# Optimization experiments

Hardware: AMD Instinct MI355X
Metric: run time of the kernel (lower is better)

The kernel has to match this reference:

```python
import jax, jax.numpy as jnp
import numpy as np

N = 50000      # nodes
E = 1600000    # edges (avg degree 32)
G = 128        # graphs in batch
NE = 5         # spectral supports (edge_attr channels)
NIN = 16       # input node features
H = 64         # nout1 hidden width
NCLS = 6
BN_EPS = 1e-5


def setup_inputs() -> dict:
    key = jax.random.key(0)
    ks = jax.random.split(key, 12)
    s = 0.1  # weight init scale
    x = jax.random.normal(ks[0], (N, NIN), dtype=jnp.float32)
    edge_index = jax.random.randint(ks[1], (2, E), 0, N, dtype=jnp.int32)
    edge_attr = jax.random.normal(ks[2], (E, NE), dtype=jnp.float32)
    # sorted segment ids covering all G graphs (non-empty segments)
    batch = ((jnp.arange(N, dtype=jnp.int32) * G) // N).astype(jnp.int32)
    W1 = jax.random.normal(ks[3], (NE, NIN, H), dtype=jnp.float32) * s
    W2 = jax.random.normal(ks[4], (NE, H, H), dtype=jnp.float32) * s
    W3 = jax.random.normal(ks[5], (NE, H, H), dtype=jnp.float32) * s
    W4 = jax.random.normal(ks[6], (NE, H, H), dtype=jnp.float32) * s
    b1 = jnp.zeros((H,), jnp.float32)
    b2 = jnp.zeros((H,), jnp.float32)
    b3 = jnp.zeros((H,), jnp.float32)
    b4 = jnp.zeros((H,), jnp.float32)
    bn_gamma = jnp.ones((2 * H,), jnp.float32)
    bn_beta = jnp.zeros((2 * H,), jnp.float32)
    bn_mean = jax.random.normal(ks[7], (2 * H,), dtype=jnp.float32)
    bn_var = jax.random.uniform(ks[8], (2 * H,), dtype=jnp.float32) + 0.5
    fc_w = jax.random.normal(ks[9], (2 * H, NCLS), dtype=jnp.float32) * s
    fc_b = jnp.zeros((NCLS,), jnp.float32)
    return {"x": x, "edge_index": edge_index, "edge_attr": edge_attr,
            "batch": batch, "W1": W1, "b1": b1, "W2": W2, "b2": b2,
            "W3": W3, "b3": b3, "W4": W4, "b4": b4,
            "bn_gamma": bn_gamma, "bn_beta": bn_beta,
            "bn_mean": bn_mean, "bn_var": bn_var,
            "fc_w": fc_w, "fc_b": fc_b}


def spect_conv(x, src, dst, edge_attr, W, b):
    # SpectConv(selfconn=False): out = sum_k scatter_add(edge_attr[:,k]*x[src] -> dst) @ W[k] + b
    xs = x[src]  # [E, F] gather
    n = x.shape[0]
    out = jnp.zeros((n, W.shape[2]), x.dtype)
    for k in range(W.shape[0]):  # K=5 spectral supports
        h = jax.ops.segment_sum(edge_attr[:, k:k + 1] * xs, dst, num_segments=n)
        out = out + h @ W[k]
    return out + b


def reference(x, edge_index, edge_attr, batch, W1, b1, W2, b2, W3, b3, W4, b4,
              bn_gamma, bn_beta, bn_mean, bn_var, fc_w, fc_b):
    src, dst = edge_index[0], edge_index[1]
    h = jax.nn.relu(spect_conv(x, src, dst, edge_attr, W1, b1))
    h = jax.nn.relu(spect_conv(h, src, dst, edge_attr, W2, b2))
    h = jax.nn.relu(spect_conv(h, src, dst, edge_attr, W3, b3))
    h = jax.nn.relu(spect_conv(h, src, dst, edge_attr, W4, b4))
    pooled = jnp.concatenate([
        jax.ops.segment_sum(h, batch, num_segments=G),
        jax.ops.segment_max(h, batch, num_segments=G)], axis=1)  # [G, 2H]
    bn = (pooled - bn_mean) * jax.lax.rsqrt(bn_var + BN_EPS) * bn_gamma + bn_beta
    return jax.nn.log_softmax(bn @ fc_w + fc_b, axis=1)
```

## Files before the change

### kernel.cpp

```cpp
#include <hip/hip_runtime.h>


#define Nn   50000
#define Ne   1600000
#define Gg   128
#define NEk  5
#define NINf 16
#define NCLSo 6
#define NB   196

using short8 = __attribute__((ext_vector_type(8))) short;
using f32x4  = __attribute__((ext_vector_type(4))) float;

__device__ __forceinline__ float2 bf2u(unsigned u) {
    return make_float2(__uint_as_float(u << 16), __uint_as_float(u & 0xffff0000u));
}
__device__ __forceinline__ unsigned f2bf(float a, float b) {
    unsigned ua = __float_as_uint(a), ub = __float_as_uint(b);
    ua += 0x7fffu + ((ua >> 16) & 1u);
    ub += 0x7fffu + ((ub >> 16) & 1u);
    return (ua >> 16) | (ub & 0xffff0000u);
}
__device__ __forceinline__ unsigned short f2bf1(float a) {
    unsigned ua = __float_as_uint(a);
    ua += 0x7fffu + ((ua >> 16) & 1u);
    return (unsigned short)(ua >> 16);
}


__global__ void k_pad_x(const float* __restrict__ x, unsigned* __restrict__ h0) {
    int i = blockIdx.x * 256 + threadIdx.x;
    if (i >= Nn * 32) return;
    int n = i >> 5, p = i & 31;
    int f0 = 2 * p;
    float v0 = (f0 < NINf) ? x[n * NINf + f0] : 0.f;
    float v1 = (f0 + 1 < NINf) ? x[n * NINf + f0 + 1] : 0.f;
    h0[i] = f2bf(v0, v1);
}

__global__ void k_pad_w1(const float* __restrict__ W1, float* __restrict__ W1p) {
    int i = blockIdx.x * 256 + threadIdx.x;
    if (i >= NEk * 64 * 64) return;
    int h = i & 63, f = (i >> 6) & 63, k = i >> 12;
    W1p[i] = (f < NINf) ? W1[(k * NINf + f) * 64 + h] : 0.f;
}

__global__ void k_pack_b(const float* __restrict__ W, unsigned short* __restrict__ bhi,
                         unsigned short* __restrict__ blo) {
    int i = blockIdx.x * 256 + threadIdx.x;
    if (i >= 20480) return;
    int j = i & 7, lane = (i >> 3) & 63, t2 = i >> 9;
    int nt = t2 / 10, kstep = t2 - nt * 10;
    int k = kstep * 32 + (lane >> 4) * 8 + j;
    int col = nt * 16 + (lane & 15);
    float v = W[k * 64 + col];
    unsigned short hi = f2bf1(v);
    float fhi = __uint_as_float(((unsigned)hi) << 16);
    bhi[i] = hi;
    blo[i] = f2bf1(v - fhi);
}

__global__ void k_rank(const int* __restrict__ ei, int* __restrict__ deg,
                       int* __restrict__ rank) {
    int e = blockIdx.x * 256 + threadIdx.x;
    if (e >= Ne) return;
    rank[e] = atomicAdd(&deg[ei[Ne + e]], 1);
}


__global__ void k_blocksum(const int* __restrict__ deg, int* __restrict__ bsum) {
    __shared__ int l[256];
    int t = threadIdx.x;
    int i = blockIdx.x * 256 + t;
    l[t] = (i < Nn) ? deg[i] : 0;
    __syncthreads();
    for (int off = 128; off > 0; off >>= 1) {
        if (t < off) l[t] += l[t + off];
        __syncthreads();
    }
    if (t == 0) bsum[blockIdx.x] = l[0];
}

__global__ void k_scanpart(const int* __restrict__ bsum, int* __restrict__ boff) {
    __shared__ int l[256];
    int t = threadIdx.x;
    int v = (t < NB) ? bsum[t] : 0;
    l[t] = v;
    __syncthreads();
    for (int off = 1; off < 256; off <<= 1) {
        int u = (t >= off) ? l[t - off] : 0;
        __syncthreads();
        l[t] += u;
        __syncthreads();
    }
    if (t < NB) boff[t] = l[t] - v;
}

__global__ void k_scanfinal(const int* __restrict__ deg, const int* __restrict__ boff,
                            int* __restrict__ rowstart) {
    __shared__ int l[256];
    int t = threadIdx.x;
    int i = blockIdx.x * 256 + t;
    int v = (i < Nn) ? deg[i] : 0;
    l[t] = v;
    __syncthreads();
    for (int off = 1; off < 256; off <<= 1) {
        int u = (t >= off) ? l[t - off] : 0;
        __syncthreads();
        l[t] += u;
        __syncthreads();
    }
    if (i <= Nn) rowstart[i] = boff[blockIdx.x] + l[t] - v;
}

__global__ void k_place(const int* __restrict__ ei, const float* __restrict__ eattr,
                        const int* __restrict__ rowstart, const int* __restrict__ rank,
                        uint4* __restrict__ recs) {
    int e = blockIdx.x * 256 + threadIdx.x;
    if (e >= Ne) return;
    int d = ei[Ne + e];
    int pos = rowstart[d] + rank[e];
    const float* a = eattr + (size_t)e * 5;
    uint4 r;
    r.x = (unsigned)ei[e];
    r.y = f2bf(a[0], a[1]);
    r.z = f2bf(a[2], a[3]);
    r.w = f2bf(a[4], 0.f);
    recs[pos] = r;
}

__global__ void k_bounds(const int* __restrict__ batch, int* __restrict__ sg,
                         int* __restrict__ eg) {
    int n = blockIdx.x * 256 + threadIdx.x;
    if (n >= Nn) return;
    int g = batch[n];
    if (n == 0) sg[g] = 0;
    else {
        int gp = batch[n - 1];
        if (gp != g) { sg[g] = n; eg[gp] = n; }
    }
    if (n == Nn - 1) eg[g] = Nn;
}


__global__ __launch_bounds__(256) void k_aggregate(
    const unsigned* __restrict__ hin, const int* __restrict__ rowstart,
    const uint4* __restrict__ recs, unsigned* __restrict__ agg) {
    int lane = threadIdx.x & 63;
    int l = lane & 31, half = lane >> 5;
    int node = __builtin_amdgcn_readfirstlane((int)(blockIdx.x * 4 + (threadIdx.x >> 6)));
    int beg = rowstart[node], end = rowstart[node + 1];
    float2 c0 = {0.f, 0.f}, c1 = c0, c2 = c0, c3 = c0, c4 = c0;
    int ee = beg;
#define EDGE(E) { \
    uint4 r = recs[(E)]; \
    unsigned hx = hin[(size_t)(int)r.x * 32 + l]; \
    float2 xv = bf2u(hx); \
    float2 A01 = bf2u(r.y), A23 = bf2u(r.z); \
    float a4v = __uint_as_float(r.w << 16); \
    c0.x = fmaf(A01.x, xv.x, c0.x); c0.y = fmaf(A01.x, xv.y, c0.y); \
    c1.x = fmaf(A01.y, xv.x, c1.x); c1.y = fmaf(A01.y, xv.y, c1.y); \
    c2.x = fmaf(A23.x, xv.x, c2.x); c2.y = fmaf(A23.x, xv.y, c2.y); \
    c3.x = fmaf(A23.y, xv.x, c3.x); c3.y = fmaf(A23.y, xv.y, c3.y); \
    c4.x = fmaf(a4v,  xv.x, c4.x); c4.y = fmaf(a4v,  xv.y, c4.y); }
    for (; ee + 8 <= end; ee += 8) {
        EDGE(ee + half) EDGE(ee + 2 + half) EDGE(ee + 4 + half) EDGE(ee + 6 + half)
    }
    for (; ee + 2 <= end; ee += 2) { EDGE(ee + half) }
    if (ee < end) { if (half == 0) { EDGE(ee) } }
#undef EDGE
    c0.x += __shfl(c0.x, lane ^ 32); c0.y += __shfl(c0.y, lane ^ 32);
    c1.x += __shfl(c1.x, lane ^ 32); c1.y += __shfl(c1.y, lane ^ 32);
    c2.x += __shfl(c2.x, lane ^ 32); c2.y += __shfl(c2.y, lane ^ 32);
    c3.x += __shfl(c3.x, lane ^ 32); c3.y += __shfl(c3.y, lane ^ 32);
    c4.x += __shfl(c4.x, lane ^ 32); c4.y += __shfl(c4.y, lane ^ 32);
    if (half == 0) {
        unsigned* o = agg + (size_t)node * 160 + l;
        o[0]   = f2bf(c0.x, c0.y);
        o[32]  = f2bf(c1.x, c1.y);
        o[64]  = f2bf(c2.x, c2.y);
        o[96]  = f2bf(c3.x, c3.y);
        o[128] = f2bf(c4.x, c4.y);
    }
}

#define SPAD 41
__global__ __launch_bounds__(256) void k_transform(
    const uint4* __restrict__ A, const unsigned short* __restrict__ bhi,
    const unsigned short* __restrict__ blo, const float* __restrict__ bias,
    unsigned* __restrict__ outh) {
    __shared__ uint4 smem[64 * SPAD];
    int t = threadIdx.x;
    int lane = t & 63, wave = t >> 6;
    int m = lane & 15, quad = lane >> 4;
    int blk = blockIdx.x;

#pragma unroll
    for (int it = 0; it < 10; ++it) {
        int v = t + it * 256;
        int row = v / 40, off = v - row * 40;
        int node = blk * 64 + row;
        if (node >= Nn) node = Nn - 1;
        smem[row * SPAD + off] = A[(size_t)node * 40 + off];
    }
    __syncthreads();

    f32x4 acc0 = {0.f, 0.f, 0.f, 0.f}, acc1 = acc0, acc2 = acc0, acc3 = acc0;
    const uint4* arow = smem + (wave * 16 + m) * SPAD + quad;
#pragma unroll 2
    for (int ks = 0; ks < 10; ++ks) {
        short8 a = *(const short8*)(arow + ks * 4);
        size_t bb = ((size_t)ks * 64 + lane) * 8;
        short8 h0 = *(const short8*)(bhi + bb);
        short8 l0 = *(const short8*)(blo + bb);
        acc0 = __builtin_amdgcn_mfma_f32_16x16x32_bf16(a, h0, acc0, 0, 0, 0);
        acc0 = __builtin_amdgcn_mfma_f32_16x16x32_bf16(a, l0, acc0, 0, 0, 0);
        short8 h1 = *(const short8*)(bhi + bb + 5120);
        short8 l1 = *(const short8*)(blo + bb + 5120);
        acc1 = __builtin_amdgcn_mfma_f32_16x16x32_bf16(a, h1, acc1, 0, 0, 0);
        acc1 = __builtin_amdgcn_mfma_f32_16x16x32_bf16(a, l1, acc1, 0, 0, 0);
        short8 h2 = *(const short8*)(bhi + bb + 10240);
        short8 l2 = *(const short8*)(blo + bb + 10240);
        acc2 = __builtin_amdgcn_mfma_f32_16x16x32_bf16(a, h2, acc2, 0, 0, 0);
        acc2 = __builtin_amdgcn_mfma_f32_16x16x32_bf16(a, l2, acc2, 0, 0, 0);
        short8 h3 = *(const short8*)(bhi + bb + 15360);
        short8 l3 = *(const short8*)(blo + bb + 15360);
        acc3 = __builtin_amdgcn_mfma_f32_16x16x32_bf16(a, h3, acc3, 0, 0, 0);
        acc3 = __builtin_amdgcn_mfma_f32_16x16x32_bf16(a, l3, acc3, 0, 0, 0);
    }
    __syncthreads();

    float* Cs = (float*)smem;
#pragma unroll
    for (int r = 0; r < 4; ++r) {
        int base = wave * 1152 + (quad * 4 + r) * 72 + m;
        Cs[base]      = acc0[r];
        Cs[base + 16] = acc1[r];
        Cs[base + 32] = acc2[r];
        Cs[base + 48] = acc3[r];
    }
    __syncthreads();

    int row = t >> 2, grp = t & 3;
    int node = blk * 64 + row;
    if (node < Nn) {
        const float* cr = Cs + (row >> 4) * 1152 + (row & 15) * 72;
        unsigned o[8];
#pragma unroll
        for (int j = 0; j < 8; ++j) {
            int pp = grp * 8 + j;
            float v0 = fmaxf(cr[2 * pp]     + bias[2 * pp],     0.f);
            float v1 = fmaxf(cr[2 * pp + 1] + bias[2 * pp + 1], 0.f);
            o[j] = f2bf(v0, v1);
        }
        uint4* dst = (uint4*)(outh + (size_t)node * 32 + grp * 8);
        dst[0] = make_uint4(o[0], o[1], o[2], o[3]);
        dst[1] = make_uint4(o[4], o[5], o[6], o[7]);
    }
}


__global__ __launch_bounds__(256) void k_pool(const unsigned* __restrict__ h,
                                              const int* __restrict__ sg,
                                              const int* __restrict__ eg,
                                              float* __restrict__ pooled) {
    __shared__ float2 ls[256], lm[256];
    int g = blockIdx.x, t = threadIdx.x;
    int p = t & 31, q = t >> 5;
    int s = sg[g], e = eg[g];
    float2 sum = {0.f, 0.f}, mx = {0.f, 0.f};
    for (int n = s + q; n < e; n += 8) {
        float2 v = bf2u(h[(size_t)n * 32 + p]);
        sum.x += v.x; sum.y += v.y;
        mx.x = fmaxf(mx.x, v.x); mx.y = fmaxf(mx.y, v.y);
    }
    ls[t] = sum; lm[t] = mx;
    __syncthreads();
    if (t < 32) {
        float2 ss = ls[t], mm = lm[t];
        for (int i = 1; i < 8; ++i) {
            float2 a = ls[t + i * 32], b = lm[t + i * 32];
            ss.x += a.x; ss.y += a.y;
            mm.x = fmaxf(mm.x, b.x); mm.y = fmaxf(mm.y, b.y);
        }
        pooled[g * 128 + 2 * t]          = ss.x;
        pooled[g * 128 + 2 * t + 1]      = ss.y;
        pooled[g * 128 + 64 + 2 * t]     = mm.x;
        pooled[g * 128 + 64 + 2 * t + 1] = mm.y;
    }
}

__global__ void k_head(const float* __restrict__ pooled, const float* __restrict__ gamma,
                       const float* __restrict__ beta, const float* __restrict__ mean,
                       const float* __restrict__ var, const float* __restrict__ fcw,
                       const float* __restrict__ fcb, float* __restrict__ out) {
    __shared__ float y[128];
    __shared__ float lg[8];
    int g = blockIdx.x, c = threadIdx.x;
    float p = pooled[g * 128 + c];
    y[c] = (p - mean[c]) * rsqrtf(var[c] + 1e-5f) * gamma[c] + beta[c];
    __syncthreads();
    if (c < NCLSo) {
        float l = fcb[c];
        for (int i = 0; i < 128; ++i) l += y[i] * fcw[i * NCLSo + c];
        lg[c] = l;
    }
    __syncthreads();
    if (c == 0) {
        float m = lg[0];
        for (int j = 1; j < NCLSo; ++j) m = fmaxf(m, lg[j]);
        float se = 0.f;
        for (int j = 0; j < NCLSo; ++j) se += expf(lg[j] - m);
        float lse = m + logf(se);
        for (int j = 0; j < NCLSo; ++j) out[g * NCLSo + j] = lg[j] - lse;
    }
}


static inline size_t rup(size_t x) { return (x + 255) & ~(size_t)255; }

extern "C" void kernel_launch(void* const* d_in, const int* in_sizes, int n_in,
                              void* d_out, int out_size, void* d_ws, size_t ws_size,
                              hipStream_t stream) {
    const float* x     = (const float*)d_in[0];
    const int*   ei    = (const int*)d_in[1];
    const float* eattr = (const float*)d_in[2];
    const int*   batch = (const int*)d_in[3];
    const float* W1    = (const float*)d_in[4];
    const float* b1    = (const float*)d_in[5];
    const float* W2    = (const float*)d_in[6];
    const float* b2    = (const float*)d_in[7];
    const float* W3    = (const float*)d_in[8];
    const float* b3    = (const float*)d_in[9];
    const float* W4    = (const float*)d_in[10];
    const float* b4    = (const float*)d_in[11];
    const float* gamma = (const float*)d_in[12];
    const float* beta  = (const float*)d_in[13];
    const float* mean  = (const float*)d_in[14];
    const float* var   = (const float*)d_in[15];
    const float* fcw   = (const float*)d_in[16];
    const float* fcb   = (const float*)d_in[17];
    float* out = (float*)d_out;

    char* p = (char*)d_ws;
    auto take = [&](size_t bytes) { char* r = p; p += rup(bytes); return r; };
    int*            deg      = (int*)take((size_t)(Nn + 1) * 4);
    int*            rowstart = (int*)take((size_t)(Nn + 1) * 4);
    int*            bsum     = (int*)take((size_t)NB * 4);
    int*            boff     = (int*)take((size_t)NB * 4);
    int*            rank     = (int*)take((size_t)Ne * 4);
    uint4*          recs     = (uint4*)take((size_t)Ne * 16);
    unsigned*       hA       = (unsigned*)take((size_t)Nn * 32 * 4);
    unsigned*       hB       = (unsigned*)take((size_t)Nn * 32 * 4);
    unsigned*       agg      = (unsigned*)take((size_t)Nn * 160 * 4);
    float*          W1p      = (float*)take((size_t)NEk * 64 * 64 * 4);
    unsigned short* bhiA     = (unsigned short*)take((size_t)4 * 20480 * 2);
    unsigned short* bloA     = (unsigned short*)take((size_t)4 * 20480 * 2);
    float*          pooled   = (float*)take((size_t)Gg * 128 * 4);
    int*            sg       = (int*)take((size_t)Gg * 4);
    int*            eg       = (int*)take((size_t)Gg * 4);

    hipMemsetAsync(deg, 0, (size_t)(Nn + 1) * 4, stream);

    k_pad_x<<<(Nn * 32 + 255) / 256, 256, 0, stream>>>(x, hA);
    k_pad_w1<<<(NEk * 64 * 64 + 255) / 256, 256, 0, stream>>>(W1, W1p);
    k_pack_b<<<80, 256, 0, stream>>>(W1p, bhiA,             bloA);
    k_pack_b<<<80, 256, 0, stream>>>(W2,  bhiA + 20480,     bloA + 20480);
    k_pack_b<<<80, 256, 0, stream>>>(W3,  bhiA + 2 * 20480, bloA + 2 * 20480);
    k_pack_b<<<80, 256, 0, stream>>>(W4,  bhiA + 3 * 20480, bloA + 3 * 20480);
    k_rank<<<(Ne + 255) / 256, 256, 0, stream>>>(ei, deg, rank);
    k_blocksum<<<NB, 256, 0, stream>>>(deg, bsum);
    k_scanpart<<<1, 256, 0, stream>>>(bsum, boff);
    k_scanfinal<<<NB, 256, 0, stream>>>(deg, boff, rowstart);
    k_place<<<(Ne + 255) / 256, 256, 0, stream>>>(ei, eattr, rowstart, rank, recs);
    k_bounds<<<(Nn + 255) / 256, 256, 0, stream>>>(batch, sg, eg);

    const float* bs[4] = { b1, b2, b3, b4 };
    unsigned* cur = hA;
    unsigned* nxt = hB;
    for (int L = 0; L < 4; ++L) {
        k_aggregate<<<Nn / 4, 256, 0, stream>>>(cur, rowstart, recs, agg);
        k_transform<<<(Nn + 63) / 64, 256, 0, stream>>>(
            (const uint4*)agg, bhiA + (size_t)L * 20480, bloA + (size_t)L * 20480,
            bs[L], nxt);
        unsigned* tmp = cur; cur = nxt; nxt = tmp;
    }

    k_pool<<<Gg, 256, 0, stream>>>(cur, sg, eg, pooled);
    k_head<<<Gg, 128, 0, stream>>>(pooled, gamma, beta, mean, var, fcw, fcb, out);
}
```

Before: 525.6 us.

## Fuse aggregation and MFMA transform into one per-layer kernel; pad degree counters

Merges the edge aggregation kernel and the bf16 MFMA transform into a single 512-thread kernel per layer. Each block aggregates 64 nodes straight into LDS, then multiplies them by the packed weights, so the 160-wide aggregate buffer no longer makes a round trip through global memory. Separately, the degree counters are spaced 64 bytes apart to cut atomic contention and false sharing in the rank pass. The trade-offs are less aggregation parallelism per block (each wave handles 8 nodes serially), a barrier that makes the MFMA stage wait for the slowest node's gather, and a 16x larger degree array to memset.

```diff
diff --git a/kernel.cpp b/kernel.cpp
--- a/kernel.cpp
+++ b/kernel.cpp
@@ -8,6 +8,7 @@
 #define NINf 16
 #define NCLSo 6
 #define NB   196
+#define SPAD 41
 
 using short8 = __attribute__((ext_vector_type(8))) short;
 using f32x4  = __attribute__((ext_vector_type(4))) float;
@@ -64,7 +65,7 @@
                        int* __restrict__ rank) {
     int e = blockIdx.x * 256 + threadIdx.x;
     if (e >= Ne) return;
-    rank[e] = atomicAdd(&deg[ei[Ne + e]], 1);
+    rank[e] = atomicAdd(&deg[ei[Ne + e] * 16], 1);
 }
 
 
@@ -72,7 +73,7 @@
     __shared__ int l[256];
     int t = threadIdx.x;
     int i = blockIdx.x * 256 + t;
-    l[t] = (i < Nn) ? deg[i] : 0;
+    l[t] = (i < Nn) ? deg[i * 16] : 0;
     __syncthreads();
     for (int off = 128; off > 0; off >>= 1) {
         if (t < off) l[t] += l[t + off];
@@ -101,7 +102,7 @@
     __shared__ int l[256];
     int t = threadIdx.x;
     int i = blockIdx.x * 256 + t;
-    int v = (i < Nn) ? deg[i] : 0;
+    int v = (i < Nn) ? deg[i * 16] : 0;
     l[t] = v;
     __syncthreads();
     for (int off = 1; off < 256; off <<= 1) {
@@ -142,16 +143,24 @@
     if (n == Nn - 1) eg[g] = Nn;
 }
 
-
-__global__ __launch_bounds__(256) void k_aggregate(
+__global__ __launch_bounds__(512) void k_layer(
     const unsigned* __restrict__ hin, const int* __restrict__ rowstart,
-    const uint4* __restrict__ recs, unsigned* __restrict__ agg) {
-    int lane = threadIdx.x & 63;
+    const uint4* __restrict__ recs, const unsigned short* __restrict__ bhi,
+    const unsigned short* __restrict__ blo, const float* __restrict__ bias,
+    unsigned* __restrict__ outh) {
+    __shared__ uint4 smem[64 * SPAD];
+    int t = threadIdx.x;
+    int lane = t & 63, wave = t >> 6;
     int l = lane & 31, half = lane >> 5;
-    int node = __builtin_amdgcn_readfirstlane((int)(blockIdx.x * 4 + (threadIdx.x >> 6)));
-    int beg = rowstart[node], end = rowstart[node + 1];
-    float2 c0 = {0.f, 0.f}, c1 = c0, c2 = c0, c3 = c0, c4 = c0;
-    int ee = beg;
+    unsigned* As = (unsigned*)smem;
+
+    for (int i = 0; i < 8; ++i) {
+        int row = wave * 8 + i;
+        int node = __builtin_amdgcn_readfirstlane(blockIdx.x * 64 + row);
+        float2 c0 = {0.f, 0.f}, c1 = c0, c2 = c0, c3 = c0, c4 = c0;
+        if (node < Nn) {
+            int beg = rowstart[node], end = rowstart[node + 1];
+            int ee = beg;
 #define EDGE(E) { \
     uint4 r = recs[(E)]; \
     unsigned hx = hin[(size_t)(int)r.x * 32 + l]; \
@@ -163,99 +172,71 @@
     c2.x = fmaf(A23.x, xv.x, c2.x); c2.y = fmaf(A23.x, xv.y, c2.y); \
     c3.x = fmaf(A23.y, xv.x, c3.x); c3.y = fmaf(A23.y, xv.y, c3.y); \
     c4.x = fmaf(a4v,  xv.x, c4.x); c4.y = fmaf(a4v,  xv.y, c4.y); }
-    for (; ee + 8 <= end; ee += 8) {
-        EDGE(ee + half) EDGE(ee + 2 + half) EDGE(ee + 4 + half) EDGE(ee + 6 + half)
-    }
-    for (; ee + 2 <= end; ee += 2) { EDGE(ee + half) }
-    if (ee < end) { if (half == 0) { EDGE(ee) } }
+            for (; ee + 8 <= end; ee += 8) {
+                EDGE(ee + half) EDGE(ee + 2 + half) EDGE(ee + 4 + half) EDGE(ee + 6 + half)
+            }
+            for (; ee + 2 <= end; ee += 2) { EDGE(ee + half) }
+            if (ee < end) { if (half == 0) { EDGE(ee) } }
 #undef EDGE
-    c0.x += __shfl(c0.x, lane ^ 32); c0.y += __shfl(c0.y, lane ^ 32);
-    c1.x += __shfl(c1.x, lane ^ 32); c1.y += __shfl(c1.y, lane ^ 32);
-    c2.x += __shfl(c2.x, lane ^ 32); c2.y += __shfl(c2.y, lane ^ 32);
-    c3.x += __shfl(c3.x, lane ^ 32); c3.y += __shfl(c3.y, lane ^ 32);
-    c4.x += __shfl(c4.x, lane ^ 32); c4.y += __shfl(c4.y, lane ^ 32);
-    if (half == 0) {
-        unsigned* o = agg + (size_t)node * 160 + l;
-        o[0]   = f2bf(c0.x, c0.y);
-        o[32]  = f2bf(c1.x, c1.y);
-        o[64]  = f2bf(c2.x, c2.y);
-        o[96]  = f2bf(c3.x, c3.y);
-        o[128] = f2bf(c4.x, c4.y);
-    }
-}
-
-#define SPAD 41
-__global__ __launch_bounds__(256) void k_transform(
-    const uint4* __restrict__ A, const unsigned short* __restrict__ bhi,
-    const unsigned short* __restrict__ blo, const float* __restrict__ bias,
-    unsigned* __restrict__ outh) {
-    __shared__ uint4 smem[64 * SPAD];
-    int t = threadIdx.x;
-    int lane = t & 63, wave = t >> 6;
+            c0.x += __shfl(c0.x, lane ^ 32); c0.y += __shfl(c0.y, lane ^ 32);
+            c1.x += __shfl(c1.x, lane ^ 32); c1.y += __shfl(c1.y, lane ^ 32);
+            c2.x += __shfl(c2.x, lane ^ 32); c2.y += __shfl(c2.y, lane ^ 32);
+            c3.x += __shfl(c3.x, lane ^ 32); c3.y += __shfl(c3.y, lane ^ 32);
+            c4.x += __shfl(c4.x, lane ^ 32); c4.y += __shfl(c4.y, lane ^ 32);
+        }
+        if (half == 0) {
+            unsigned* o = As + row * (SPAD * 4) + l;
+            o[0]   = f2bf(c0.x, c0.y);
+            o[32]  = f2bf(c1.x, c1.y);
+            o[64]  = f2bf(c2.x, c2.y);
+            o[96]  = f2bf(c3.x, c3.y);
+            o[128] = f2bf(c4.x, c4.y);
+        }
+    }
+    __syncthreads();
+
     int m = lane & 15, quad = lane >> 4;
-    int blk = blockIdx.x;
-
-#pragma unroll
-    for (int it = 0; it < 10; ++it) {
-        int v = t + it * 256;
-        int row = v / 40, off = v - row * 40;
-        int node = blk * 64 + row;
-        if (node >= Nn) node = Nn - 1;
-        smem[row * SPAD + off] = A[(size_t)node * 40 + off];
-    }
-    __syncthreads();
-
-    f32x4 acc0 = {0.f, 0.f, 0.f, 0.f}, acc1 = acc0, acc2 = acc0, acc3 = acc0;
-    const uint4* arow = smem + (wave * 16 + m) * SPAD + quad;
+    int mtile = wave & 3, np = wave >> 2;
+    f32x4 acc0 = {0.f, 0.f, 0.f, 0.f}, acc1 = acc0;
+    const uint4* arow = smem + (mtile * 16 + m) * SPAD + quad;
 #pragma unroll 2
     for (int ks = 0; ks < 10; ++ks) {
         short8 a = *(const short8*)(arow + ks * 4);
-        size_t bb = ((size_t)ks * 64 + lane) * 8;
-        short8 h0 = *(const short8*)(bhi + bb);
-        short8 l0 = *(const short8*)(blo + bb);
+        size_t b0 = ((size_t)((2 * np) * 10 + ks) * 64 + lane) * 8;
+        size_t b1 = ((size_t)((2 * np + 1) * 10 + ks) * 64 + lane) * 8;
+        short8 h0 = *(const short8*)(bhi + b0);
+        short8 l0 = *(const short8*)(blo + b0);
         acc0 = __builtin_amdgcn_mfma_f32_16x16x32_bf16(a, h0, acc0, 0, 0, 0);
         acc0 = __builtin_amdgcn_mfma_f32_16x16x32_bf16(a, l0, acc0, 0, 0, 0);
-        short8 h1 = *(const short8*)(bhi + bb + 5120);
-        short8 l1 = *(const short8*)(blo + bb + 5120);
+        short8 h1 = *(const short8*)(bhi + b1);
+        short8 l1 = *(const short8*)(blo + b1);
         acc1 = __builtin_amdgcn_mfma_f32_16x16x32_bf16(a, h1, acc1, 0, 0, 0);
         acc1 = __builtin_amdgcn_mfma_f32_16x16x32_bf16(a, l1, acc1, 0, 0, 0);
-        short8 h2 = *(const short8*)(bhi + bb + 10240);
-        short8 l2 = *(const short8*)(blo + bb + 10240);
-        acc2 = __builtin_amdgcn_mfma_f32_16x16x32_bf16(a, h2, acc2, 0, 0, 0);
-        acc2 = __builtin_amdgcn_mfma_f32_16x16x32_bf16(a, l2, acc2, 0, 0, 0);
-        short8 h3 = *(const short8*)(bhi + bb + 15360);
-        short8 l3 = *(const short8*)(blo + bb + 15360);
-        acc3 = __builtin_amdgcn_mfma_f32_16x16x32_bf16(a, h3, acc3, 0, 0, 0);
-        acc3 = __builtin_amdgcn_mfma_f32_16x16x32_bf16(a, l3, acc3, 0, 0, 0);
     }
     __syncthreads();
 
     float* Cs = (float*)smem;
 #pragma unroll
     for (int r = 0; r < 4; ++r) {
-        int base = wave * 1152 + (quad * 4 + r) * 72 + m;
-        Cs[base]      = acc0[r];
-        Cs[base + 16] = acc1[r];
-        Cs[base + 32] = acc2[r];
-        Cs[base + 48] = acc3[r];
-    }
-    __syncthreads();
-
-    int row = t >> 2, grp = t & 3;
-    int node = blk * 64 + row;
+        int row = mtile * 16 + quad * 4 + r;
+        Cs[row * 66 + (2 * np) * 16 + m]     = acc0[r];
+        Cs[row * 66 + (2 * np + 1) * 16 + m] = acc1[r];
+    }
+    __syncthreads();
+
+    int row = t >> 3, cg = t & 7;
+    int node = blockIdx.x * 64 + row;
     if (node < Nn) {
-        const float* cr = Cs + (row >> 4) * 1152 + (row & 15) * 72;
-        unsigned o[8];
+        const float* cr = Cs + row * 66 + cg * 8;
+        const float* bb = bias + cg * 8;
+        unsigned o[4];
 #pragma unroll
-        for (int j = 0; j < 8; ++j) {
-            int pp = grp * 8 + j;
-            float v0 = fmaxf(cr[2 * pp]     + bias[2 * pp],     0.f);
-            float v1 = fmaxf(cr[2 * pp + 1] + bias[2 * pp + 1], 0.f);
+        for (int j = 0; j < 4; ++j) {
+            float v0 = fmaxf(cr[2 * j]     + bb[2 * j],     0.f);
+            float v1 = fmaxf(cr[2 * j + 1] + bb[2 * j + 1], 0.f);
             o[j] = f2bf(v0, v1);
         }
-        uint4* dst = (uint4*)(outh + (size_t)node * 32 + grp * 8);
-        dst[0] = make_uint4(o[0], o[1], o[2], o[3]);
-        dst[1] = make_uint4(o[4], o[5], o[6], o[7]);
+        *(uint4*)(outh + (size_t)node * 32 + cg * 4) = make_uint4(o[0], o[1], o[2], o[3]);
     }
 }
 
@@ -344,7 +325,7 @@
 
     char* p = (char*)d_ws;
     auto take = [&](size_t bytes) { char* r = p; p += rup(bytes); return r; };
-    int*            deg      = (int*)take((size_t)(Nn + 1) * 4);
+    int*            deg      = (int*)take((size_t)(Nn + 1) * 64);
     int*            rowstart = (int*)take((size_t)(Nn + 1) * 4);
     int*            bsum     = (int*)take((size_t)NB * 4);
     int*            boff     = (int*)take((size_t)NB * 4);
@@ -352,7 +333,6 @@
     uint4*          recs     = (uint4*)take((size_t)Ne * 16);
     unsigned*       hA       = (unsigned*)take((size_t)Nn * 32 * 4);
     unsigned*       hB       = (unsigned*)take((size_t)Nn * 32 * 4);
-    unsigned*       agg      = (unsigned*)take((size_t)Nn * 160 * 4);
     float*          W1p      = (float*)take((size_t)NEk * 64 * 64 * 4);
     unsigned short* bhiA     = (unsigned short*)take((size_t)4 * 20480 * 2);
     unsigned short* bloA     = (unsigned short*)take((size_t)4 * 20480 * 2);
@@ -360,7 +340,7 @@
     int*            sg       = (int*)take((size_t)Gg * 4);
     int*            eg       = (int*)take((size_t)Gg * 4);
 
-    hipMemsetAsync(deg, 0, (size_t)(Nn + 1) * 4, stream);
+    hipMemsetAsync(deg, 0, (size_t)(Nn + 1) * 64, stream);
 
     k_pad_x<<<(Nn * 32 + 255) / 256, 256, 0, stream>>>(x, hA);
     k_pad_w1<<<(NEk * 64 * 64 + 255) / 256, 256, 0, stream>>>(W1, W1p);
@@ -379,9 +359,8 @@
     unsigned* cur = hA;
     unsigned* nxt = hB;
     for (int L = 0; L < 4; ++L) {
-        k_aggregate<<<Nn / 4, 256, 0, stream>>>(cur, rowstart, recs, agg);
-        k_transform<<<(Nn + 63) / 64, 256, 0, stream>>>(
-            (const uint4*)agg, bhiA + (size_t)L * 20480, bloA + (size_t)L * 20480,
+        k_layer<<<(Nn + 63) / 64, 512, 0, stream>>>(
+            cur, rowstart, recs, bhiA + (size_t)L * 20480, bloA + (size_t)L * 20480,
             bs[L], nxt);
         unsigned* tmp = cur; cur = nxt; nxt = tmp;
     }
```

Result: slower. 603.7 us (+14.8%).

## Split node features into two halves and aggregate each in a separate pass

Applied to the files above, without the earlier changes.

Node features are stored as two 32-feature bf16 arrays (lo/hi), and aggregation runs twice per layer, once per half. Each pass uses a 16-lane feature slice with four edges in flight per wave, so each gathered feature table is half the size and more likely to stay in cache. The edge records are read twice per layer, now with nontemporal loads. The degree counters are also spaced 64 bytes apart to reduce atomic contention on shared cache lines.

```diff
diff --git a/kernel.cpp b/kernel.cpp
--- a/kernel.cpp
+++ b/kernel.cpp
@@ -8,9 +8,11 @@
 #define NINf 16
 #define NCLSo 6
 #define NB   196
+#define SPAD 41
 
 using short8 = __attribute__((ext_vector_type(8))) short;
 using f32x4  = __attribute__((ext_vector_type(4))) float;
+using uint4v = __attribute__((ext_vector_type(4))) unsigned;
 
 __device__ __forceinline__ float2 bf2u(unsigned u) {
     return make_float2(__uint_as_float(u << 16), __uint_as_float(u & 0xffff0000u));
@@ -28,14 +30,17 @@
 }
 
 
-__global__ void k_pad_x(const float* __restrict__ x, unsigned* __restrict__ h0) {
+__global__ void k_pad_x(const float* __restrict__ x, unsigned* __restrict__ hLo,
+                        unsigned* __restrict__ hHi) {
     int i = blockIdx.x * 256 + threadIdx.x;
     if (i >= Nn * 32) return;
     int n = i >> 5, p = i & 31;
     int f0 = 2 * p;
     float v0 = (f0 < NINf) ? x[n * NINf + f0] : 0.f;
     float v1 = (f0 + 1 < NINf) ? x[n * NINf + f0 + 1] : 0.f;
-    h0[i] = f2bf(v0, v1);
+    unsigned v = f2bf(v0, v1);
+    if (p < 16) hLo[n * 16 + p] = v;
+    else        hHi[n * 16 + (p - 16)] = v;
 }
 
 __global__ void k_pad_w1(const float* __restrict__ W1, float* __restrict__ W1p) {
@@ -64,7 +69,7 @@
                        int* __restrict__ rank) {
     int e = blockIdx.x * 256 + threadIdx.x;
     if (e >= Ne) return;
-    rank[e] = atomicAdd(&deg[ei[Ne + e]], 1);
+    rank[e] = atomicAdd(&deg[ei[Ne + e] * 16], 1);
 }
 
 
@@ -72,7 +77,7 @@
     __shared__ int l[256];
     int t = threadIdx.x;
     int i = blockIdx.x * 256 + t;
-    l[t] = (i < Nn) ? deg[i] : 0;
+    l[t] = (i < Nn) ? deg[i * 16] : 0;
     __syncthreads();
     for (int off = 128; off > 0; off >>= 1) {
         if (t < off) l[t] += l[t + off];
@@ -101,7 +106,7 @@
     __shared__ int l[256];
     int t = threadIdx.x;
     int i = blockIdx.x * 256 + t;
-    int v = (i < Nn) ? deg[i] : 0;
+    int v = (i < Nn) ? deg[i * 16] : 0;
     l[t] = v;
     __syncthreads();
     for (int off = 1; off < 256; off <<= 1) {
@@ -143,18 +148,18 @@
 }
 
 
-__global__ __launch_bounds__(256) void k_aggregate(
+__global__ __launch_bounds__(256) void k_aggregate_half(
     const unsigned* __restrict__ hin, const int* __restrict__ rowstart,
-    const uint4* __restrict__ recs, unsigned* __restrict__ agg) {
+    const uint4v* __restrict__ recs, unsigned* __restrict__ agg, int halfSel) {
     int lane = threadIdx.x & 63;
-    int l = lane & 31, half = lane >> 5;
+    int l = lane & 15, q = lane >> 4;
     int node = __builtin_amdgcn_readfirstlane((int)(blockIdx.x * 4 + (threadIdx.x >> 6)));
     int beg = rowstart[node], end = rowstart[node + 1];
     float2 c0 = {0.f, 0.f}, c1 = c0, c2 = c0, c3 = c0, c4 = c0;
     int ee = beg;
 #define EDGE(E) { \
-    uint4 r = recs[(E)]; \
-    unsigned hx = hin[(size_t)(int)r.x * 32 + l]; \
+    uint4v r = __builtin_nontemporal_load(&recs[(E)]); \
+    unsigned hx = hin[(size_t)(int)r.x * 16 + l]; \
     float2 xv = bf2u(hx); \
     float2 A01 = bf2u(r.y), A23 = bf2u(r.z); \
     float a4v = __uint_as_float(r.w << 16); \
@@ -163,19 +168,25 @@
     c2.x = fmaf(A23.x, xv.x, c2.x); c2.y = fmaf(A23.x, xv.y, c2.y); \
     c3.x = fmaf(A23.y, xv.x, c3.x); c3.y = fmaf(A23.y, xv.y, c3.y); \
     c4.x = fmaf(a4v,  xv.x, c4.x); c4.y = fmaf(a4v,  xv.y, c4.y); }
-    for (; ee + 8 <= end; ee += 8) {
-        EDGE(ee + half) EDGE(ee + 2 + half) EDGE(ee + 4 + half) EDGE(ee + 6 + half)
-    }
-    for (; ee + 2 <= end; ee += 2) { EDGE(ee + half) }
-    if (ee < end) { if (half == 0) { EDGE(ee) } }
+    for (; ee + 16 <= end; ee += 16) {
+        EDGE(ee + q) EDGE(ee + 4 + q) EDGE(ee + 8 + q) EDGE(ee + 12 + q)
+    }
+    for (; ee + 4 <= end; ee += 4) { EDGE(ee + q) }
+    int rem = end - ee;
+    if (q < rem) { EDGE(ee + q) }
 #undef EDGE
+    c0.x += __shfl(c0.x, lane ^ 16); c0.y += __shfl(c0.y, lane ^ 16);
+    c1.x += __shfl(c1.x, lane ^ 16); c1.y += __shfl(c1.y, lane ^ 16);
+    c2.x += __shfl(c2.x, lane ^ 16); c2.y += __shfl(c2.y, lane ^ 16);
+    c3.x += __shfl(c3.x, lane ^ 16); c3.y += __shfl(c3.y, lane ^ 16);
+    c4.x += __shfl(c4.x, lane ^ 16); c4.y += __shfl(c4.y, lane ^ 16);
     c0.x += __shfl(c0.x, lane ^ 32); c0.y += __shfl(c0.y, lane ^ 32);
     c1.x += __shfl(c1.x, lane ^ 32); c1.y += __shfl(c1.y, lane ^ 32);
     c2.x += __shfl(c2.x, lane ^ 32); c2.y += __shfl(c2.y, lane ^ 32);
     c3.x += __shfl(c3.x, lane ^ 32); c3.y += __shfl(c3.y, lane ^ 32);
     c4.x += __shfl(c4.x, lane ^ 32); c4.y += __shfl(c4.y, lane ^ 32);
-    if (half == 0) {
-        unsigned* o = agg + (size_t)node * 160 + l;
+    if (q == 0) {
+        unsigned* o = agg + (size_t)node * 160 + halfSel * 16 + l;
         o[0]   = f2bf(c0.x, c0.y);
         o[32]  = f2bf(c1.x, c1.y);
         o[64]  = f2bf(c2.x, c2.y);
@@ -184,11 +195,10 @@
     }
 }
 
-#define SPAD 41
 __global__ __launch_bounds__(256) void k_transform(
     const uint4* __restrict__ A, const unsigned short* __restrict__ bhi,
     const unsigned short* __restrict__ blo, const float* __restrict__ bias,
-    unsigned* __restrict__ outh) {
+    unsigned* __restrict__ outLo, unsigned* __restrict__ outHi) {
     __shared__ uint4 smem[64 * SPAD];
     int t = threadIdx.x;
     int lane = t & 63, wave = t >> 6;
@@ -253,14 +263,16 @@
             float v1 = fmaxf(cr[2 * pp + 1] + bias[2 * pp + 1], 0.f);
             o[j] = f2bf(v0, v1);
         }
-        uint4* dst = (uint4*)(outh + (size_t)node * 32 + grp * 8);
+        unsigned* dstArr = (grp < 2) ? outLo : outHi;
+        uint4* dst = (uint4*)(dstArr + (size_t)node * 16 + (grp & 1) * 8);
         dst[0] = make_uint4(o[0], o[1], o[2], o[3]);
         dst[1] = make_uint4(o[4], o[5], o[6], o[7]);
     }
 }
 
 
-__global__ __launch_bounds__(256) void k_pool(const unsigned* __restrict__ h,
+__global__ __launch_bounds__(256) void k_pool(const unsigned* __restrict__ hLo,
+                                              const unsigned* __restrict__ hHi,
                                               const int* __restrict__ sg,
                                               const int* __restrict__ eg,
                                               float* __restrict__ pooled) {
@@ -268,9 +280,11 @@
     int g = blockIdx.x, t = threadIdx.x;
     int p = t & 31, q = t >> 5;
     int s = sg[g], e = eg[g];
+    const unsigned* harr = (p < 16) ? hLo : hHi;
+    int po = p & 15;
     float2 sum = {0.f, 0.f}, mx = {0.f, 0.f};
     for (int n = s + q; n < e; n += 8) {
-        float2 v = bf2u(h[(size_t)n * 32 + p]);
+        float2 v = bf2u(harr[(size_t)n * 16 + po]);
         sum.x += v.x; sum.y += v.y;
         mx.x = fmaxf(mx.x, v.x); mx.y = fmaxf(mx.y, v.y);
     }
@@ -344,14 +358,16 @@
 
     char* p = (char*)d_ws;
     auto take = [&](size_t bytes) { char* r = p; p += rup(bytes); return r; };
-    int*            deg      = (int*)take((size_t)(Nn + 1) * 4);
+    int*            deg      = (int*)take((size_t)(Nn + 1) * 64);
     int*            rowstart = (int*)take((size_t)(Nn + 1) * 4);
     int*            bsum     = (int*)take((size_t)NB * 4);
     int*            boff     = (int*)take((size_t)NB * 4);
     int*            rank     = (int*)take((size_t)Ne * 4);
     uint4*          recs     = (uint4*)take((size_t)Ne * 16);
-    unsigned*       hA       = (unsigned*)take((size_t)Nn * 32 * 4);
-    unsigned*       hB       = (unsigned*)take((size_t)Nn * 32 * 4);
+    unsigned*       hLoA     = (unsigned*)take((size_t)Nn * 16 * 4);
+    unsigned*       hHiA     = (unsigned*)take((size_t)Nn * 16 * 4);
+    unsigned*       hLoB     = (unsigned*)take((size_t)Nn * 16 * 4);
+    unsigned*       hHiB     = (unsigned*)take((size_t)Nn * 16 * 4);
     unsigned*       agg      = (unsigned*)take((size_t)Nn * 160 * 4);
     float*          W1p      = (float*)take((size_t)NEk * 64 * 64 * 4);
     unsigned short* bhiA     = (unsigned short*)take((size_t)4 * 20480 * 2);
@@ -360,9 +376,9 @@
     int*            sg       = (int*)take((size_t)Gg * 4);
     int*            eg       = (int*)take((size_t)Gg * 4);
 
-    hipMemsetAsync(deg, 0, (size_t)(Nn + 1) * 4, stream);
-
-    k_pad_x<<<(Nn * 32 + 255) / 256, 256, 0, stream>>>(x, hA);
+    (void)hipMemsetAsync(deg, 0, (size_t)(Nn + 1) * 64, stream);
+
+    k_pad_x<<<(Nn * 32 + 255) / 256, 256, 0, stream>>>(x, hLoA, hHiA);
     k_pad_w1<<<(NEk * 64 * 64 + 255) / 256, 256, 0, stream>>>(W1, W1p);
     k_pack_b<<<80, 256, 0, stream>>>(W1p, bhiA,             bloA);
     k_pack_b<<<80, 256, 0, stream>>>(W2,  bhiA + 20480,     bloA + 20480);
@@ -376,16 +392,19 @@
     k_bounds<<<(Nn + 255) / 256, 256, 0, stream>>>(batch, sg, eg);
 
     const float* bs[4] = { b1, b2, b3, b4 };
-    unsigned* cur = hA;
-    unsigned* nxt = hB;
+    unsigned *curLo = hLoA, *curHi = hHiA, *nxtLo = hLoB, *nxtHi = hHiB;
     for (int L = 0; L < 4; ++L) {
-        k_aggregate<<<Nn / 4, 256, 0, stream>>>(cur, rowstart, recs, agg);
+        k_aggregate_half<<<Nn / 4, 256, 0, stream>>>(curLo, rowstart,
+                                                     (const uint4v*)recs, agg, 0);
+        k_aggregate_half<<<Nn / 4, 256, 0, stream>>>(curHi, rowstart,
+                                                     (const uint4v*)recs, agg, 1);
         k_transform<<<(Nn + 63) / 64, 256, 0, stream>>>(
             (const uint4*)agg, bhiA + (size_t)L * 20480, bloA + (size_t)L * 20480,
-            bs[L], nxt);
-        unsigned* tmp = cur; cur = nxt; nxt = tmp;
-    }
-
-    k_pool<<<Gg, 256, 0, stream>>>(cur, sg, eg, pooled);
+            bs[L], nxtLo, nxtHi);
+        unsigned* t0 = curLo; curLo = nxtLo; nxtLo = t0;
+        unsigned* t1 = curHi; curHi = nxtHi; nxtHi = t1;
+    }
+
+    k_pool<<<Gg, 256, 0, stream>>>(curLo, curHi, sg, eg, pooled);
     k_head<<<Gg, 128, 0, stream>>>(pooled, gamma, beta, mean, var, fcw, fcb, out);
 }
```

Result: slower. 667.3 us (+27.0%).
